# Performance work log

Hardware: AMD Instinct MI355X
Metric: run time of the kernel (lower is better)

The kernel has to match this reference:

```python
import jax, jax.numpy as jnp
import numpy as np

B, T, D, H, L = 64, 512, 1024, 1024, 4


def setup_inputs() -> dict:
    key = jax.random.key(0)
    ks = jax.random.split(key, 5)
    scale = 1.0 / np.sqrt(H)
    return {
        "x": jax.random.normal(ks[0], (B, T, D), dtype=jnp.float32),
        "Wih": jax.random.normal(ks[1], (L, 4 * H, D), dtype=jnp.float32) * scale,
        "Whh": jax.random.normal(ks[2], (L, 4 * H, H), dtype=jnp.float32) * scale,
        "bih": jax.random.normal(ks[3], (L, 4 * H), dtype=jnp.float32) * scale,
        "bhh": jax.random.normal(ks[4], (L, 4 * H), dtype=jnp.float32) * scale,
    }


def _lstm_layer(x_tbd, Wih, Whh, b):
    # x_tbd: [T, B, in]; Wih: [4H, in]; Whh: [4H, H]; b: [4H]
    Bsz = x_tbd.shape[1]
    Hsz = Whh.shape[1]
    # precompute the input-side GEMM for the whole sequence in one shot
    xg = jnp.einsum('tbd,gd->tbg', x_tbd, Wih) + b  # [T, B, 4H]

    def step(carry, xg_t):
        h, c = carry
        z = xg_t + h @ Whh.T  # [B, 4H]
        i, f, g, o = jnp.split(z, 4, axis=-1)  # torch LSTMCell gate order
        c = jax.nn.sigmoid(f) * c + jax.nn.sigmoid(i) * jnp.tanh(g)
        h = jax.nn.sigmoid(o) * jnp.tanh(c)
        return (h, c), h

    init = (jnp.zeros((Bsz, Hsz), x_tbd.dtype), jnp.zeros((Bsz, Hsz), x_tbd.dtype))
    (h_last, _), hs = jax.lax.scan(step, init, xg)
    return hs, h_last  # hs: [T, B, H]


def reference(x, Wih, Whh, bih, bhh):
    # layer-by-layer over the stack (fixed small L); each layer scans over time
    seq = jnp.transpose(x, (1, 0, 2))  # [T, B, D]
    h_last = None
    for l in range(L):
        seq, h_last = _lstm_layer(seq, Wih[l], Whh[l], bih[l] + bhh[l])
    return h_last  # [B, output_size], hidden of last layer at final timestep
```

## Files before the change

kernel.cpp:

```cpp
#include <hip/hip_runtime.h>
#include <math.h>


#define BSZ 64
#define TSZ 512
#define DSZ 1024
#define HSZ 1024
#define LSZ 4
#define NBLK 256
#define NTHR 512
#define NSTEP (TSZ + LSZ - 1)
#define BUFB 32768

typedef _Float16 half8  __attribute__((ext_vector_type(8)));
typedef _Float16 half4  __attribute__((ext_vector_type(4)));
typedef _Float16 half2v __attribute__((ext_vector_type(2)));
typedef float    f32x4  __attribute__((ext_vector_type(4)));
typedef float    f32x8  __attribute__((ext_vector_type(8)));

constexpr size_t N_X  = (size_t)BSZ * TSZ * DSZ;
constexpr size_t N_H  = (size_t)2 * LSZ * BSZ * HSZ;
constexpr size_t OFF_X     = 0;
constexpr size_t OFF_H     = OFF_X + N_X * 2;
constexpr size_t OFF_FLAGS = OFF_H + N_H * 2;
constexpr size_t BAR_BYTES = (size_t)NBLK * 64;

__device__ inline float fsig(float x) {
  return __builtin_amdgcn_rcpf(1.0f + __expf(-x));
}
__device__ inline float ftanh(float x) {
  float e = __expf(fminf(2.0f * x, 80.0f));
  return 1.0f - 2.0f * __builtin_amdgcn_rcpf(e + 1.0f);
}

__device__ inline void gload16(const void* g, void* l) {
  __builtin_amdgcn_global_load_lds(
      (const __attribute__((address_space(1))) void*)g,
      (__attribute__((address_space(3))) void*)l, 16, 0, 0);
}

__device__ inline void gbar(unsigned* flags, unsigned tgt) {
  __syncthreads();
  const int t = threadIdx.x;
  if (t == 0)
    __hip_atomic_store(&flags[(size_t)blockIdx.x * 16], tgt, __ATOMIC_RELAXED,
                       __HIP_MEMORY_SCOPE_AGENT);
  if (t < NBLK) {
    while (__hip_atomic_load(&flags[(size_t)t * 16], __ATOMIC_RELAXED,
                             __HIP_MEMORY_SCOPE_AGENT) < tgt)
      __builtin_amdgcn_s_sleep(2);
  }
  __syncthreads();
  if (t == 0) __builtin_amdgcn_fence(__ATOMIC_ACQUIRE, "agent");
  __syncthreads();
}

__global__ __launch_bounds__(NTHR, 1) void lstm_persistent(
    const float* __restrict__ xin, const float* __restrict__ Wih,
    const float* __restrict__ Whh, const float* __restrict__ bih,
    const float* __restrict__ bhh, float* __restrict__ out,
    char* __restrict__ ws)
{
  _Float16* x16   = (_Float16*)(ws + OFF_X);
  _Float16* h16   = (_Float16*)(ws + OFF_H);
  unsigned* flags = (unsigned*)(ws + OFF_FLAGS);

  const int tid  = threadIdx.x;
  const int gtid = blockIdx.x * NTHR + tid;
  const int lane = tid & 63;
  const int w    = tid >> 6;
  const int mat  = w >> 2;
  const int rp   = (w >> 1) & 1;
  const int kh   = w & 1;
  const int ln15 = lane & 15;
  const int lq   = lane >> 4;

  const int l  = blockIdx.x >> 6;
  const int cc = blockIdx.x & 63;
  const int c0 = cc * 16;

  const float* Wsel = mat ? Whh : Wih;
  half8 bw[2][16];
#pragma unroll
  for (int gl = 0; gl < 2; ++gl) {
    const float* wrow =
        Wsel + (size_t)(l * 4096 + (rp * 2 + gl) * 1024 + c0 + ln15) * 1024 +
        kh * 512;
#pragma unroll
    for (int ks = 0; ks < 16; ++ks) {
      f32x8 f = *(const f32x8*)(wrow + ks * 32 + lq * 8);
      bw[gl][ks] = __builtin_convertvector(f, half8);
    }
  }

  const int gb = tid >> 3;
  const int gc = (tid & 7) * 2;
  float bsg[4][2];
#pragma unroll
  for (int g = 0; g < 4; ++g) {
    const int bb = l * 4096 + g * 1024 + c0 + gc;
    bsg[g][0] = bih[bb] + bhh[bb];
    bsg[g][1] = bih[bb + 1] + bhh[bb + 1];
  }
  float cr0 = 0.f, cr1 = 0.f;

  const int sb   = tid >> 3;
  const int pswl = ((tid & 7) ^ (sb & 7)) << 4;
  const int dstb = (tid >> 6) << 10;

  {
    const f32x4* s4 = (const f32x4*)xin;
    unsigned long long* xu = (unsigned long long*)x16;
    for (int i = gtid; i < (int)(N_X / 4); i += NBLK * NTHR) {
      half4 v = __builtin_convertvector(s4[i], half4);
      __hip_atomic_store(&xu[i], __builtin_bit_cast(unsigned long long, v),
                         __ATOMIC_RELAXED, __HIP_MEMORY_SCOPE_AGENT);
    }
    unsigned long long* hz = (unsigned long long*)h16;
    for (int i = gtid; i < (int)(N_H / 4); i += NBLK * NTHR)
      __hip_atomic_store(&hz[i], 0ull, __ATOMIC_RELAXED,
                         __HIP_MEMORY_SCOPE_AGENT);
  }
  unsigned btgt = 1;
  gbar(flags, btgt++);

  __shared__ __align__(16) char smem[2 * BUFB];
  float* pl = (float*)smem;

  const int lm1 = (l > 0) ? (l - 1) : 0;

  for (int s = 0; s < NSTEP; ++s) {
    const int t = s - l;
    if (t >= 0 && t < TSZ) {
      const int prevslot = (s + 1) & 1;
      const _Float16* hin  = h16 + (size_t)prevslot * (LSZ * BSZ * HSZ) +
                             (size_t)lm1 * (BSZ * HSZ);
      const _Float16* hown = h16 + (size_t)prevslot * (LSZ * BSZ * HSZ) +
                             (size_t)l * (BSZ * HSZ);
      const _Float16* base0 = (l == 0) ? x16 + (size_t)t * DSZ : hin;
      const size_t    str0  = (l == 0) ? (size_t)TSZ * DSZ : (size_t)HSZ;

      const char* p0 = (const char*)(base0 + (size_t)sb * str0) + pswl;
      const char* p1 = (const char*)(hown + (size_t)sb * HSZ) + pswl;

      auto stage = [&](int kc, int bsel) {
        const char* r0 = p0 + kc * 128;
        const char* r1 = p1 + kc * 128;
        char* d = smem + bsel * BUFB + dstb;
        gload16(r0,        d);
        gload16(r0 + 1024, d + 8192);
        gload16(r1,        d + 16384);
        gload16(r1 + 1024, d + 24576);
      };

      f32x4 acc[4][2] = {};

      stage(0, 0);
      __syncthreads();

      const int rdoff = mat * 16384 + kh * 8192;
#pragma unroll
      for (int kc = 0; kc < 8; ++kc) {
        if (kc < 7) stage(kc + 1, (kc + 1) & 1);
        const char* rdb = smem + (kc & 1) * BUFB + rdoff;
#pragma unroll
        for (int ksl = 0; ksl < 2; ++ksl) {
#pragma unroll
          for (int mt = 0; mt < 4; ++mt) {
            const int row = mt * 16 + ln15;
            const half8 a = *(const half8*)(rdb + row * 128 +
                                            ((ksl * 64 + lq * 16) ^
                                             ((row & 7) << 4)));
            acc[mt][0] = __builtin_amdgcn_mfma_f32_16x16x32_f16(
                a, bw[0][kc * 2 + ksl], acc[mt][0], 0, 0, 0);
            acc[mt][1] = __builtin_amdgcn_mfma_f32_16x16x32_f16(
                a, bw[1][kc * 2 + ksl], acc[mt][1], 0, 0, 0);
          }
        }
        __syncthreads();
      }

      if (mat == 0) {
#pragma unroll
        for (int mt = 0; mt < 4; ++mt)
#pragma unroll
          for (int gl = 0; gl < 2; ++gl) {
            const int v  = (rp * 2 + gl) * 16 + ln15;
            const int bp = (mt * 16 + lq * 4) ^ ((ln15 & 7) << 2);
            *(f32x4*)&pl[kh * 4096 + v * 64 + bp] = acc[mt][gl];
          }
      }
      __syncthreads();
      if (mat == 1) {
#pragma unroll
        for (int mt = 0; mt < 4; ++mt)
#pragma unroll
          for (int gl = 0; gl < 2; ++gl) {
            const int v  = (rp * 2 + gl) * 16 + ln15;
            const int bp = (mt * 16 + lq * 4) ^ ((ln15 & 7) << 2);
            f32x4* p = (f32x4*)&pl[kh * 4096 + v * 64 + bp];
            *p = *p + acc[mt][gl];
          }
      }
      __syncthreads();

      {
        float z[4][2];
#pragma unroll
        for (int g = 0; g < 4; ++g)
#pragma unroll
          for (int j = 0; j < 2; ++j) {
            const int v  = g * 16 + gc + j;
            const int bp = gb ^ ((v & 7) << 2);
            z[g][j] = pl[0 * 4096 + v * 64 + bp] +
                      pl[1 * 4096 + v * 64 + bp] + bsg[g][j];
          }
        float cn0 = fsig(z[1][0]) * cr0 + fsig(z[0][0]) * ftanh(z[2][0]);
        float cn1 = fsig(z[1][1]) * cr1 + fsig(z[0][1]) * ftanh(z[2][1]);
        float hn0 = fsig(z[3][0]) * ftanh(cn0);
        float hn1 = fsig(z[3][1]) * ftanh(cn1);
        cr0 = cn0; cr1 = cn1;
        half2v hv; hv[0] = (_Float16)hn0; hv[1] = (_Float16)hn1;
        const size_t ho = (size_t)(s & 1) * (LSZ * BSZ * HSZ) +
                          (size_t)l * (BSZ * HSZ) + (size_t)gb * HSZ + c0 + gc;
        __hip_atomic_store((unsigned*)(h16 + ho),
                           __builtin_bit_cast(unsigned, hv),
                           __ATOMIC_RELAXED, __HIP_MEMORY_SCOPE_AGENT);
        if (l == LSZ - 1 && t == TSZ - 1) {
          out[(size_t)gb * HSZ + c0 + gc]     = hn0;
          out[(size_t)gb * HSZ + c0 + gc + 1] = hn1;
        }
      }
    }
    gbar(flags, btgt++);
  }
}

extern "C" void kernel_launch(void* const* d_in, const int* in_sizes, int n_in,
                              void* d_out, int out_size, void* d_ws, size_t ws_size,
                              hipStream_t stream) {
  const float* x   = (const float*)d_in[0];
  const float* Wih = (const float*)d_in[1];
  const float* Whh = (const float*)d_in[2];
  const float* bih = (const float*)d_in[3];
  const float* bhh = (const float*)d_in[4];
  float* out = (float*)d_out;
  char*  ws  = (char*)d_ws;

  hipMemsetAsync(ws + OFF_FLAGS, 0, BAR_BYTES, stream);

  void* args[] = {(void*)&x, (void*)&Wih, (void*)&Whh, (void*)&bih,
                  (void*)&bhh, (void*)&out, (void*)&ws};
  hipLaunchCooperativeKernel((const void*)lstm_persistent, dim3(NBLK), dim3(NTHR),
                             args, 0, stream);
}
```

Before: 4.811 ms.

## Split K four ways per wave so each A fragment feeds all four gates

Each wave now covers all four gate rows for a quarter of K, instead of two gates over half of K. Every A fragment read from LDS is reused across four MFMAs rather than two, which halves LDS reads per MFMA. The staging layout changes to contiguous 64-byte chunks per K quarter, and the final reduction sums four partial slabs instead of two. The unswizzled LDS layout may bring back bank conflicts, and the extra partial sums add work in the epilogue.

After: 6.065 ms. 1.26x slower.

```diff
diff --git a/kernel.cpp b/kernel.cpp
--- a/kernel.cpp
+++ b/kernel.cpp
@@ -70,8 +70,7 @@
   const int lane = tid & 63;
   const int w    = tid >> 6;
   const int mat  = w >> 2;
-  const int rp   = (w >> 1) & 1;
-  const int kh   = w & 1;
+  const int kq   = w & 3;
   const int ln15 = lane & 15;
   const int lq   = lane >> 4;
 
@@ -80,16 +79,15 @@
   const int c0 = cc * 16;
 
   const float* Wsel = mat ? Whh : Wih;
-  half8 bw[2][16];
-#pragma unroll
-  for (int gl = 0; gl < 2; ++gl) {
+  half8 bw[4][8];
+#pragma unroll
+  for (int g = 0; g < 4; ++g) {
     const float* wrow =
-        Wsel + (size_t)(l * 4096 + (rp * 2 + gl) * 1024 + c0 + ln15) * 1024 +
-        kh * 512;
-#pragma unroll
-    for (int ks = 0; ks < 16; ++ks) {
-      f32x8 f = *(const f32x8*)(wrow + ks * 32 + lq * 8);
-      bw[gl][ks] = __builtin_convertvector(f, half8);
+        Wsel + (size_t)(l * 4096 + g * 1024 + c0 + ln15) * 1024 + kq * 256;
+#pragma unroll
+    for (int kc = 0; kc < 8; ++kc) {
+      f32x8 f = *(const f32x8*)(wrow + kc * 32 + lq * 8);
+      bw[g][kc] = __builtin_convertvector(f, half8);
     }
   }
 
@@ -104,8 +102,9 @@
   }
   float cr0 = 0.f, cr1 = 0.f;
 
-  const int sb   = tid >> 3;
-  const int pswl = ((tid & 7) ^ (sb & 7)) << 4;
+  const int sb   = (tid & 255) >> 2;
+  const int ssl  = (tid & 3) << 4;
+  const int hi   = tid >> 8;
   const int dstb = (tid >> 6) << 10;
 
   {
@@ -140,43 +139,40 @@
       const _Float16* base0 = (l == 0) ? x16 + (size_t)t * DSZ : hin;
       const size_t    str0  = (l == 0) ? (size_t)TSZ * DSZ : (size_t)HSZ;
 
-      const char* p0 = (const char*)(base0 + (size_t)sb * str0) + pswl;
-      const char* p1 = (const char*)(hown + (size_t)sb * HSZ) + pswl;
+      const char* p0 = (const char*)(base0 + (size_t)sb * str0) + ssl;
+      const char* p1 = (const char*)(hown + (size_t)sb * HSZ) + ssl;
 
       auto stage = [&](int kc, int bsel) {
-        const char* r0 = p0 + kc * 128;
-        const char* r1 = p1 + kc * 128;
         char* d = smem + bsel * BUFB + dstb;
-        gload16(r0,        d);
-        gload16(r0 + 1024, d + 8192);
-        gload16(r1,        d + 16384);
-        gload16(r1 + 1024, d + 24576);
+        const int kb = kc * 64;
+#pragma unroll
+        for (int it = 0; it < 4; ++it) {
+          const char* src = (it >> 1 ? p1 : p0) +
+                            (((2 * it + hi) & 3) << 9) + kb;
+          gload16(src, d + it * 8192);
+        }
       };
 
-      f32x4 acc[4][2] = {};
+      f32x4 acc[4][4] = {};
 
       stage(0, 0);
       __syncthreads();
 
-      const int rdoff = mat * 16384 + kh * 8192;
+      const int rdoff = (mat * 4 + kq) * 4096;
 #pragma unroll
       for (int kc = 0; kc < 8; ++kc) {
         if (kc < 7) stage(kc + 1, (kc + 1) & 1);
-        const char* rdb = smem + (kc & 1) * BUFB + rdoff;
-#pragma unroll
-        for (int ksl = 0; ksl < 2; ++ksl) {
-#pragma unroll
-          for (int mt = 0; mt < 4; ++mt) {
-            const int row = mt * 16 + ln15;
-            const half8 a = *(const half8*)(rdb + row * 128 +
-                                            ((ksl * 64 + lq * 16) ^
-                                             ((row & 7) << 4)));
-            acc[mt][0] = __builtin_amdgcn_mfma_f32_16x16x32_f16(
-                a, bw[0][kc * 2 + ksl], acc[mt][0], 0, 0, 0);
-            acc[mt][1] = __builtin_amdgcn_mfma_f32_16x16x32_f16(
-                a, bw[1][kc * 2 + ksl], acc[mt][1], 0, 0, 0);
-          }
-        }
+        const char* sec = smem + (kc & 1) * BUFB + rdoff;
+        half8 a[4];
+#pragma unroll
+        for (int mt = 0; mt < 4; ++mt)
+          a[mt] = *(const half8*)(sec + (mt * 16 + ln15) * 64 + lq * 16);
+#pragma unroll
+        for (int g = 0; g < 4; ++g)
+#pragma unroll
+          for (int mt = 0; mt < 4; ++mt)
+            acc[mt][g] = __builtin_amdgcn_mfma_f32_16x16x32_f16(
+                a[mt], bw[g][kc], acc[mt][g], 0, 0, 0);
         __syncthreads();
       }
 
@@ -184,10 +180,10 @@
 #pragma unroll
         for (int mt = 0; mt < 4; ++mt)
 #pragma unroll
-          for (int gl = 0; gl < 2; ++gl) {
-            const int v  = (rp * 2 + gl) * 16 + ln15;
+          for (int g = 0; g < 4; ++g) {
+            const int v  = g * 16 + ln15;
             const int bp = (mt * 16 + lq * 4) ^ ((ln15 & 7) << 2);
-            *(f32x4*)&pl[kh * 4096 + v * 64 + bp] = acc[mt][gl];
+            *(f32x4*)&pl[kq * 4096 + v * 64 + bp] = acc[mt][g];
           }
       }
       __syncthreads();
@@ -195,11 +191,11 @@
 #pragma unroll
         for (int mt = 0; mt < 4; ++mt)
 #pragma unroll
-          for (int gl = 0; gl < 2; ++gl) {
-            const int v  = (rp * 2 + gl) * 16 + ln15;
+          for (int g = 0; g < 4; ++g) {
+            const int v  = g * 16 + ln15;
             const int bp = (mt * 16 + lq * 4) ^ ((ln15 & 7) << 2);
-            f32x4* p = (f32x4*)&pl[kh * 4096 + v * 64 + bp];
-            *p = *p + acc[mt][gl];
+            f32x4* p = (f32x4*)&pl[kq * 4096 + v * 64 + bp];
+            *p = *p + acc[mt][g];
           }
       }
       __syncthreads();
@@ -213,7 +209,9 @@
             const int v  = g * 16 + gc + j;
             const int bp = gb ^ ((v & 7) << 2);
             z[g][j] = pl[0 * 4096 + v * 64 + bp] +
-                      pl[1 * 4096 + v * 64 + bp] + bsg[g][j];
+                      pl[1 * 4096 + v * 64 + bp] +
+                      pl[2 * 4096 + v * 64 + bp] +
+                      pl[3 * 4096 + v * 64 + bp] + bsg[g][j];
           }
         float cn0 = fsig(z[1][0]) * cr0 + fsig(z[0][0]) * ftanh(z[2][0]);
         float cn1 = fsig(z[1][1]) * cr1 + fsig(z[0][1]) * ftanh(z[2][1]);
```
